# Optimization experiments

Measured on AMD Instinct MI355X. Metric: run time of the kernel, lower is better.

Reference implementation:

```python
import jax, jax.numpy as jnp
import numpy as np
from jax import lax

DROPOUT_RATE = 0.1  # config['dropout']


def setup_inputs() -> dict:
    key = jax.random.key(0)
    kx, kl, kwi, kwh = jax.random.split(key, 4)
    B, T, D, H = 64, 2048, 256, 256
    datamat = jax.random.normal(kx, (B, T, D), dtype=jnp.float32)
    datalens = jax.random.randint(kl, (B,), 1, T + 1, dtype=jnp.int32)
    # OptimizedLSTMCell params: combined input/hidden kernels, gate order (i, f, g, o)
    s_i = 1.0 / np.sqrt(D)
    s_h = 1.0 / np.sqrt(H)
    Wi = jax.random.uniform(kwi, (D, 4 * H), jnp.float32, -s_i, s_i)
    Wh = jax.random.uniform(kwh, (H, 4 * H), jnp.float32, -s_h, s_h)
    b = jnp.zeros((4 * H,), dtype=jnp.float32)
    return {"datamat": datamat, "Wi": Wi, "Wh": Wh, "b": b, "datalens": datalens}


def _dropout(x, rate):
    # training=True dropout with a fixed key (deterministic reference)
    keep = jax.random.bernoulli(jax.random.key(42), 1.0 - rate, x.shape)
    return jnp.where(keep, x / (1.0 - rate), jnp.zeros_like(x))


def _lstm_forward(x, Wi, Wh, b, datalens):
    # x: [B, T, D]
    B, T, D = x.shape
    H = Wh.shape[0]

    def step(carry, xt):
        c, h = carry
        z = xt @ Wi + h @ Wh + b  # [B, 4H], gate order i, f, g, o
        i, f, g, o = jnp.split(z, 4, axis=-1)
        c_new = jax.nn.sigmoid(f) * c + jax.nn.sigmoid(i) * jnp.tanh(g)
        h_new = jax.nn.sigmoid(o) * jnp.tanh(c_new)
        return (c_new, h_new), (c_new, h_new)

    c0 = jnp.zeros((B, H), dtype=x.dtype)
    h0 = jnp.zeros((B, H), dtype=x.dtype)
    _, (cs, hs) = lax.scan(step, (c0, h0), jnp.swapaxes(x, 0, 1))  # [T, B, H] each
    outputs = jnp.swapaxes(hs, 0, 1)  # [B, T, H]
    # flax nn.RNN with seq_lengths + return_carry: select carry at t = len-1 per batch
    idx = jnp.clip(datalens.astype(jnp.int32) - 1, 0, T - 1)  # [B]
    bidx = jnp.arange(B)
    c_last = cs[idx, bidx]  # [B, H]
    h_last = hs[idx, bidx]  # [B, H]
    return (c_last, h_last), outputs


def reference(datamat, Wi, Wh, b, datalens):
    x = _dropout(datamat, DROPOUT_RATE)
    out_carry, outputs = _lstm_forward(x, Wi, Wh, b, datalens)
    return (out_carry, outputs)
```

## Files before the change

### kernel.cpp

```cpp
#include <hip/hip_runtime.h>


typedef __attribute__((ext_vector_type(8))) short short8;
typedef __attribute__((ext_vector_type(4))) float floatx4;
typedef __attribute__((ext_vector_type(4))) int int4v;
typedef __attribute__((ext_vector_type(4))) unsigned short us4;
typedef __attribute__((ext_vector_type(2))) unsigned int uint2v;

#define LOG2E 1.44269504088896f

__device__ __forceinline__ unsigned short f2bf(float f) {
  unsigned int u = __float_as_uint(f);
  u = u + 0x7fffu + ((u >> 16) & 1u);
  return (unsigned short)(u >> 16);
}
__device__ __forceinline__ float fexp2(float x) { return __builtin_amdgcn_exp2f(x); }
__device__ __forceinline__ float frcp(float x) { return __builtin_amdgcn_rcpf(x); }

__device__ __forceinline__ unsigned int tf_bits(unsigned int x0, unsigned int x1) {
  const unsigned int K0 = 0u, K1 = 42u;
  const unsigned int KX = K0 ^ K1 ^ 0x1BD11BDAu;
  x0 += K0; x1 += K1;
#define TF_R(r) { x0 += x1; x1 = (x1 << (r)) | (x1 >> (32 - (r))); x1 ^= x0; }
  TF_R(13) TF_R(15) TF_R(26) TF_R(6)   x0 += K1; x1 += KX + 1u;
  TF_R(17) TF_R(29) TF_R(16) TF_R(24)  x0 += KX; x1 += K0 + 2u;
  TF_R(13) TF_R(15) TF_R(26) TF_R(6)   x0 += K0; x1 += K1 + 3u;
  TF_R(17) TF_R(29) TF_R(16) TF_R(24)  x0 += K1; x1 += KX + 4u;
  TF_R(13) TF_R(15) TF_R(26) TF_R(6)   x0 += KX; x1 += K0 + 5u;
#undef TF_R
  return x0 ^ x1;
}

__global__ __launch_bounds__(256) void k_dropout(const float* __restrict__ x,
                                                 unsigned short* __restrict__ xd) {
  const unsigned int base = (blockIdx.x * 256u + threadIdx.x) * 4u;
  const float4 xv = *reinterpret_cast<const float4*>(x + base);
  const float xs[4] = {xv.x, xv.y, xv.z, xv.w};
  us4 o;
#pragma unroll
  for (int j = 0; j < 4; ++j) {
    const unsigned int bits = tf_bits(0u, base + (unsigned int)j);
    const float u = __uint_as_float((bits >> 9) | 0x3f800000u) - 1.0f;
    const float v = (u < 0.9f) ? (xs[j] / 0.9f) : 0.0f;
    o[j] = f2bf(v);
  }
  *reinterpret_cast<us4*>(xd + base) = o;
}

__global__ __launch_bounds__(256) void k_pack_wi(const float* __restrict__ wi,
                                                 unsigned short* __restrict__ wit) {
  __shared__ float tile[32][33];
  const int k0 = blockIdx.x * 32, n0 = blockIdx.y * 32;
  const int tx = threadIdx.x & 31, ty = threadIdx.x >> 5;
#pragma unroll
  for (int i = 0; i < 4; ++i)
    tile[ty + i * 8][tx] = wi[(k0 + ty + i * 8) * 1024 + n0 + tx];
  __syncthreads();
#pragma unroll
  for (int i = 0; i < 4; ++i)
    wit[(n0 + ty + i * 8) * 256 + k0 + tx] = f2bf(tile[tx][ty + i * 8]);
}

__global__ __launch_bounds__(256) void k_colscale(const float* __restrict__ wh,
                                                  float* __restrict__ dq,
                                                  float* __restrict__ qs) {
  __shared__ float red[256];
  const int t = threadIdx.x;
  const int n = blockIdx.x * 16 + (t & 15);
  const int kg = t >> 4;
  float m = 0.f;
#pragma unroll
  for (int i = 0; i < 16; ++i)
    m = fmaxf(m, fabsf(wh[(kg * 16 + i) * 1024 + n]));
  red[t] = m;
  __syncthreads();
  if (t < 16) {
    const int nn = blockIdx.x * 16 + t;
    float mm = red[t];
#pragma unroll
    for (int j = 1; j < 16; ++j) mm = fmaxf(mm, red[t + j * 16]);
    const float s = (mm > 0.f) ? mm : 1.f;
    const float gsc[4] = {LOG2E, -LOG2E, 2.f * LOG2E, LOG2E};
    dq[nn] = (s / 16129.0f) * gsc[nn >> 8];
    qs[nn] = 127.0f / s;
  }
}

__global__ __launch_bounds__(256) void k_pack_wh_i8(const float* __restrict__ wh,
                                                    const float* __restrict__ qs,
                                                    signed char* __restrict__ wq) {
  const int tid = blockIdx.x * 256 + threadIdx.x;
  const int j = tid & 15, l = (tid >> 4) & 63, kt = (tid >> 10) & 3, ntg = tid >> 12;
  const int k = kt * 64 + ((l >> 4) << 4) + j;
  const int n = ntg * 16 + (l & 15);
  float v = rintf(wh[k * 1024 + n] * qs[n]);
  v = fminf(fmaxf(v, -127.f), 127.f);
  wq[tid] = (signed char)(int)v;
}

__global__ __launch_bounds__(512, 2) void k_fused(
    const unsigned short* __restrict__ xd, const unsigned short* __restrict__ wit,
    const float* __restrict__ bias, unsigned short* __restrict__ xp,
    const signed char* __restrict__ wq, const float* __restrict__ dq,
    const int* __restrict__ lens, float* __restrict__ out,
    unsigned int* __restrict__ flags) {
  __shared__ __align__(16) unsigned short SH[45056];

  const int tid = threadIdx.x, lane = tid & 63;

  if (blockIdx.x >= 32) {
    const int gb = (int)blockIdx.x - 32;
    const int tc = gb >> 9;
    const int rem = gb & 511;
    const int b = rem >> 3, y = rem & 7;
    const int m0 = b * 2048 + tc * 128;

    const int wv = tid >> 6;
    const int wm = wv >> 2;
    const int wn = wv & 3;
    const int srow = tid >> 2, sseg = tid & 3;
    const unsigned short* gA = xd + (m0 + srow) * 256 + sseg * 8;
    const int nsrc = ((srow >> 5) << 8) + y * 32 + (srow & 31);
    const unsigned short* gB = wit + nsrc * 256 + sseg * 8;
    const int soff = srow * 40 + sseg * 8;

    const floatx4 zero4 = {0.f, 0.f, 0.f, 0.f};
    floatx4 acc[4][2];
#pragma unroll
    for (int i = 0; i < 4; ++i) { acc[i][0] = zero4; acc[i][1] = zero4; }

    short8 ra = *(const short8*)(gA);
    short8 rb = *(const short8*)(gB);
    *(short8*)&SH[soff] = ra;
    *(short8*)&SH[10240 + soff] = rb;
    __syncthreads();

    const int frow = (lane & 15) * 40 + ((lane >> 4) << 3);
#pragma unroll 1
    for (int kt = 0; kt < 8; ++kt) {
      const int boff = (kt & 1) * 5120;
      if (kt < 7) {
        ra = *(const short8*)(gA + (kt + 1) * 32);
        rb = *(const short8*)(gB + (kt + 1) * 32);
      }
      short8 af[4], bfv[2];
#pragma unroll
      for (int mt = 0; mt < 4; ++mt)
        af[mt] = *(const short8*)&SH[boff + (wm * 64 + mt * 16) * 40 + frow];
#pragma unroll
      for (int nt = 0; nt < 2; ++nt)
        bfv[nt] = *(const short8*)&SH[10240 + boff + (wn * 32 + nt * 16) * 40 + frow];
#pragma unroll
      for (int mt = 0; mt < 4; ++mt)
#pragma unroll
        for (int nt = 0; nt < 2; ++nt)
          acc[mt][nt] = __builtin_amdgcn_mfma_f32_16x16x32_bf16(af[mt], bfv[nt], acc[mt][nt], 0, 0, 0);
      if (kt < 7) {
        const int noff = boff ^ 5120;
        *(short8*)&SH[noff + soff] = ra;
        *(short8*)&SH[10240 + noff + soff] = rb;
      }
      __syncthreads();
    }

    const float gsc[4] = {LOG2E, -LOG2E, 2.f * LOG2E, LOG2E};
    const float gv = gsc[wn];
    float bv[2];
#pragma unroll
    for (int nt = 0; nt < 2; ++nt)
      bv[nt] = bias[wn * 256 + y * 32 + nt * 16 + (lane & 15)];

    __syncthreads();
#pragma unroll
    for (int mt = 0; mt < 4; ++mt)
#pragma unroll
      for (int nt = 0; nt < 2; ++nt) {
        const int jj = wn * 32 + nt * 16 + (lane & 15);
#pragma unroll
        for (int q = 0; q < 4; ++q) {
          const int row = wm * 64 + mt * 16 + ((lane >> 4) << 2) + q;
          SH[row * 132 + jj] = f2bf((acc[mt][nt][q] + bv[nt]) * gv);
        }
      }
    __syncthreads();

#pragma unroll
    for (int k = 0; k < 8; ++k) {
      const int pi = k * 512 + tid;
      const int row = pi >> 5, u = pi & 31;
      us4 o = {SH[row * 132 + u], SH[row * 132 + 32 + u],
               SH[row * 132 + 64 + u], SH[row * 132 + 96 + u]};
      const int m = m0 + row;
      unsigned short* p = xp + ((size_t)(m & 2047) * 64 + (m >> 11)) * 1024 +
                          (size_t)(y * 32 + u) * 4;
      const uint2v ov = {(unsigned int)(unsigned short)o[0] | ((unsigned int)(unsigned short)o[1] << 16),
                         (unsigned int)(unsigned short)o[2] | ((unsigned int)(unsigned short)o[3] << 16)};
      asm volatile("global_store_dwordx2 %0, %1, off sc0 sc1"
                   :: "v"(p), "v"(ov) : "memory");
    }

    asm volatile("s_waitcnt vmcnt(0)" ::: "memory");
    __syncthreads();
    if (tid == 0) atomicAdd(&flags[tc], 1u);
    return;
  }

  signed char* As = (signed char*)SH;

  const int v = tid >> 6;
  const int wg = (int)blockIdx.x, b0 = wg * 2;

  const int4v zacc = {0, 0, 0, 0};
  ((int4v*)As)[tid] = zacc;

  int4v w[4][2][4];
#pragma unroll
  for (int g = 0; g < 4; ++g)
#pragma unroll
    for (int p = 0; p < 2; ++p)
#pragma unroll
      for (int kt = 0; kt < 4; ++kt) {
        const int ntg = g * 16 + v * 2 + p;
        w[g][p][kt] = *(const int4v*)(wq + (size_t)(((ntg * 4 + kt) * 64 + lane)) * 16);
      }

  const int r = (lane >> 4) & 1;
  const int ph = lane >> 5;
  const int u = v * 32 + ph * 16 + (lane & 15);

  float dq0 = dq[u], dq1 = dq[256 + u], dq2 = dq[512 + u], dq3 = dq[768 + u];
  const int lenm = lens[b0 + r] - 1;
  float c = 0.f, ckeep = 0.f, hkeep = 0.f;

  const signed char* AsR = As + lane * 16;
  signed char* AsW = As + ((u >> 6) * 1024 + (((u >> 4) & 3) * 16 + r * 4) * 16 + (u & 15));

  const char* xpb = (const char*)xp;
  unsigned int xoff = ((unsigned int)(b0 + r) * 1024u + (unsigned int)u * 4u) * 2u;
  char* outb = (char*)(out + 32768);
  unsigned int ooff = ((unsigned int)(b0 + r) * 524288u + (unsigned int)u) * 4u;

  if (tid == 0) {
    while (__hip_atomic_load(&flags[0], __ATOMIC_ACQUIRE, __HIP_MEMORY_SCOPE_AGENT) < 512u)
      __builtin_amdgcn_s_sleep(8);
  }
  __syncthreads();

  uint2 xcur = *(const uint2*)(xpb + xoff);
  xoff += 131072u;
  uint2 xnxt = *(const uint2*)(xpb + xoff);
  xoff += 131072u;

  __syncthreads();

#define GATES(XPAIR, WOFF0, WOFF1)                                              \
  {                                                                             \
    const float xi = __uint_as_float(XPAIR.x << 16);                            \
    const float xf = __uint_as_float(XPAIR.x & 0xffff0000u);                    \
    const float xg = __uint_as_float(XPAIR.y << 16);                            \
    const float xo = __uint_as_float(XPAIR.y & 0xffff0000u);                    \
    const int ai = ph ? acc[0][1][0] : acc[0][0][0];                            \
    const int af_ = ph ? acc[1][1][0] : acc[1][0][0];                           \
    const int ag = ph ? acc[2][1][0] : acc[2][0][0];                            \
    const int ao = ph ? acc[3][1][0] : acc[3][0][0];                            \
    const float zi = fminf(fmaf((float)ai, dq0, xi), 28.85f);                   \
    const float zf = fmaf((float)af_, dq1, xf);                                 \
    const float zg = fminf(fmaf((float)ag, dq2, xg), 57.71f);                   \
    const float zo = fminf(fmaf((float)ao, dq3, xo), 28.85f);                   \
    const float ei = fexp2(zi);                                                 \
    const float e2g = fexp2(zg);                                                \
    const float ef = fexp2(zf);                                                 \
    const float eo = fexp2(zo);                                                 \
    const float p1 = ei * (e2g - 1.f) * frcp((ei + 1.f) * (e2g + 1.f));         \
    const float cn = fmaf(frcp(1.f + ef), c, p1);                               \
    c = cn;                                                                     \
    const float e2c = fexp2(fminf(cn, 15.f) * (2.f * LOG2E));                   \
    const float h = eo * (e2c - 1.f) * frcp((eo + 1.f) * (e2c + 1.f));          \
    const float hm = fmaf(h, 127.f, 12582912.f);                                \
    AsW[WOFF0] = (signed char)__float_as_uint(hm);                              \
    AsW[WOFF1] = (signed char)__float_as_uint(hm);                              \
    *(float*)(outb + ooff) = h;                                                 \
    ooff += 1024u;                                                              \
    if (t_ == lenm) { ckeep = cn; hkeep = h; }                                  \
  }

#define MFMA_BLOCK(O0, O1, O2, O3)                                              \
  int4v acc[4][2];                                                              \
  {                                                                             \
    const int4v a0 = *(const int4v*)(AsR + (O0));                               \
    const int4v a1 = *(const int4v*)(AsR + (O1));                               \
    const int4v a2 = *(const int4v*)(AsR + (O2));                               \
    const int4v a3 = *(const int4v*)(AsR + (O3));                               \
    _Pragma("unroll") for (int g = 0; g < 4; ++g)                               \
    _Pragma("unroll") for (int p = 0; p < 2; ++p) {                             \
      acc[g][p] = __builtin_amdgcn_mfma_i32_16x16x64_i8(a0, w[g][p][0], zacc, 0, 0, 0); \
      acc[g][p] = __builtin_amdgcn_mfma_i32_16x16x64_i8(a1, w[g][p][1], acc[g][p], 0, 0, 0); \
      acc[g][p] = __builtin_amdgcn_mfma_i32_16x16x64_i8(a2, w[g][p][2], acc[g][p], 0, 0, 0); \
      acc[g][p] = __builtin_amdgcn_mfma_i32_16x16x64_i8(a3, w[g][p][3], acc[g][p], 0, 0, 0); \
    }                                                                           \
  }

#pragma unroll 1
  for (int it = 0; it < 1024; ++it) {
    if ((it & 63) == 0) {
      const int ch0 = (it >> 6) + 1;
      const int ch = ch0 < 15 ? ch0 : 15;
      if (tid == 0) {
        while (__hip_atomic_load(&flags[ch], __ATOMIC_ACQUIRE, __HIP_MEMORY_SCOPE_AGENT) < 512u)
          __builtin_amdgcn_s_sleep(8);
      }
      __syncthreads();
    }
    {
      const int t_ = 2 * it;
      const uint2 xpre = *(const uint2*)(xpb + xoff);
      xoff += 131072u;
      MFMA_BLOCK(0, 1024, 2048, 3072)
      GATES(xcur, 4096, 4224)
      xcur = xnxt;
      xnxt = xpre;
      __syncthreads();
    }
    {
      const int t_ = 2 * it + 1;
      const uint2 xpre = *(const uint2*)(xpb + xoff);
      xoff += 131072u;
      MFMA_BLOCK(4096, 5120, 6144, 7168)
      GATES(xcur, 0, 128)
      xcur = xnxt;
      xnxt = xpre;
      __syncthreads();
    }
  }
#undef GATES
#undef MFMA_BLOCK

  out[(size_t)(b0 + r) * 256 + u] = ckeep;
  out[16384 + (size_t)(b0 + r) * 256 + u] = hkeep;
}

extern "C" void kernel_launch(void* const* d_in, const int* in_sizes, int n_in,
                              void* d_out, int out_size, void* d_ws, size_t ws_size,
                              hipStream_t stream) {
  (void)in_sizes; (void)n_in; (void)out_size; (void)ws_size;
  const float* x = (const float*)d_in[0];
  const float* wi = (const float*)d_in[1];
  const float* wh = (const float*)d_in[2];
  const float* bias = (const float*)d_in[3];
  const int* lens = (const int*)d_in[4];
  float* out = (float*)d_out;

  char* ws = (char*)d_ws;
  unsigned short* xd = (unsigned short*)ws;
  unsigned short* xp = (unsigned short*)(ws + 67108864ull);
  unsigned short* wit = (unsigned short*)(ws + 335544320ull);
  float* dq = (float*)(ws + 336068608ull);
  float* qs = (float*)(ws + 336072704ull);
  signed char* wqb = (signed char*)(ws + 336076800ull);
  unsigned int* flags = (unsigned int*)(ws + 336338944ull);

  hipMemsetAsync(flags, 0, 64, stream);
  k_pack_wi<<<dim3(8, 32), 256, 0, stream>>>(wi, wit);
  k_colscale<<<64, 256, 0, stream>>>(wh, dq, qs);
  k_pack_wh_i8<<<1024, 256, 0, stream>>>(wh, qs, wqb);
  k_dropout<<<32768, 256, 0, stream>>>(x, xd);
  k_fused<<<8224, 512, 0, stream>>>(xd, wit, bias, xp, wqb, dq, lens, out, flags);
}
```

Measured before the change: 1.507 ms.

## Fold dropout into fused kernel with per-time-chunk flags and merge prep kernels

```diff
diff --git a/kernel.cpp b/kernel.cpp
--- a/kernel.cpp
+++ b/kernel.cpp
@@ -6,6 +6,7 @@
 typedef __attribute__((ext_vector_type(4))) int int4v;
 typedef __attribute__((ext_vector_type(4))) unsigned short us4;
 typedef __attribute__((ext_vector_type(2))) unsigned int uint2v;
+typedef __attribute__((ext_vector_type(4))) unsigned int uint4v;
 
 #define LOG2E 1.44269504088896f
 
@@ -31,26 +32,37 @@
   return x0 ^ x1;
 }
 
-__global__ __launch_bounds__(256) void k_dropout(const float* __restrict__ x,
-                                                 unsigned short* __restrict__ xd) {
-  const unsigned int base = (blockIdx.x * 256u + threadIdx.x) * 4u;
-  const float4 xv = *reinterpret_cast<const float4*>(x + base);
-  const float xs[4] = {xv.x, xv.y, xv.z, xv.w};
-  us4 o;
-#pragma unroll
-  for (int j = 0; j < 4; ++j) {
-    const unsigned int bits = tf_bits(0u, base + (unsigned int)j);
-    const float u = __uint_as_float((bits >> 9) | 0x3f800000u) - 1.0f;
-    const float v = (u < 0.9f) ? (xs[j] / 0.9f) : 0.0f;
-    o[j] = f2bf(v);
-  }
-  *reinterpret_cast<us4*>(xd + base) = o;
-}
-
-__global__ __launch_bounds__(256) void k_pack_wi(const float* __restrict__ wi,
-                                                 unsigned short* __restrict__ wit) {
+__global__ __launch_bounds__(256) void k_prep(const float* __restrict__ wi,
+                                              const float* __restrict__ wh,
+                                              unsigned short* __restrict__ wit,
+                                              float* __restrict__ dq,
+                                              float* __restrict__ qs) {
+  if (blockIdx.x < 64) {
+    __shared__ float red[256];
+    const int t = threadIdx.x;
+    const int n = blockIdx.x * 16 + (t & 15);
+    const int kg = t >> 4;
+    float m = 0.f;
+#pragma unroll
+    for (int i = 0; i < 16; ++i)
+      m = fmaxf(m, fabsf(wh[(kg * 16 + i) * 1024 + n]));
+    red[t] = m;
+    __syncthreads();
+    if (t < 16) {
+      const int nn = blockIdx.x * 16 + t;
+      float mm = red[t];
+#pragma unroll
+      for (int j = 1; j < 16; ++j) mm = fmaxf(mm, red[t + j * 16]);
+      const float s = (mm > 0.f) ? mm : 1.f;
+      const float gsc[4] = {LOG2E, -LOG2E, 2.f * LOG2E, LOG2E};
+      dq[nn] = (s / 16129.0f) * gsc[nn >> 8];
+      qs[nn] = 127.0f / s;
+    }
+    return;
+  }
   __shared__ float tile[32][33];
-  const int k0 = blockIdx.x * 32, n0 = blockIdx.y * 32;
+  const int idx = (int)blockIdx.x - 64;
+  const int k0 = (idx & 7) * 32, n0 = (idx >> 3) * 32;
   const int tx = threadIdx.x & 31, ty = threadIdx.x >> 5;
 #pragma unroll
   for (int i = 0; i < 4; ++i)
@@ -59,31 +71,6 @@
 #pragma unroll
   for (int i = 0; i < 4; ++i)
     wit[(n0 + ty + i * 8) * 256 + k0 + tx] = f2bf(tile[tx][ty + i * 8]);
-}
-
-__global__ __launch_bounds__(256) void k_colscale(const float* __restrict__ wh,
-                                                  float* __restrict__ dq,
-                                                  float* __restrict__ qs) {
-  __shared__ float red[256];
-  const int t = threadIdx.x;
-  const int n = blockIdx.x * 16 + (t & 15);
-  const int kg = t >> 4;
-  float m = 0.f;
-#pragma unroll
-  for (int i = 0; i < 16; ++i)
-    m = fmaxf(m, fabsf(wh[(kg * 16 + i) * 1024 + n]));
-  red[t] = m;
-  __syncthreads();
-  if (t < 16) {
-    const int nn = blockIdx.x * 16 + t;
-    float mm = red[t];
-#pragma unroll
-    for (int j = 1; j < 16; ++j) mm = fmaxf(mm, red[t + j * 16]);
-    const float s = (mm > 0.f) ? mm : 1.f;
-    const float gsc[4] = {LOG2E, -LOG2E, 2.f * LOG2E, LOG2E};
-    dq[nn] = (s / 16129.0f) * gsc[nn >> 8];
-    qs[nn] = 127.0f / s;
-  }
 }
 
 __global__ __launch_bounds__(256) void k_pack_wh_i8(const float* __restrict__ wh,
@@ -99,21 +86,62 @@
 }
 
 __global__ __launch_bounds__(512, 2) void k_fused(
-    const unsigned short* __restrict__ xd, const unsigned short* __restrict__ wit,
-    const float* __restrict__ bias, unsigned short* __restrict__ xp,
-    const signed char* __restrict__ wq, const float* __restrict__ dq,
-    const int* __restrict__ lens, float* __restrict__ out,
-    unsigned int* __restrict__ flags) {
+    const float* __restrict__ x, unsigned short* __restrict__ xd,
+    const unsigned short* __restrict__ wit, const float* __restrict__ bias,
+    unsigned short* __restrict__ xp, const signed char* __restrict__ wq,
+    const float* __restrict__ dq, const int* __restrict__ lens,
+    float* __restrict__ out, unsigned int* __restrict__ flags) {
   __shared__ __align__(16) unsigned short SH[45056];
 
   const int tid = threadIdx.x, lane = tid & 63;
 
-  if (blockIdx.x >= 32) {
-    const int gb = (int)blockIdx.x - 32;
+  if (blockIdx.x >= 32 && blockIdx.x < 8224) {
+    const int db = (int)blockIdx.x - 32;
+    const int tc = db >> 9, j = db & 511;
+    const int rloc = tid >> 5;
+    const int e0 = (tid & 31) * 8;
+    const int gr = j * 16 + rloc;
+    const int b = gr >> 7, i = gr & 127;
+    const int m = b * 2048 + tc * 128 + i;
+    const unsigned int n0 = (unsigned int)m * 256u + (unsigned int)e0;
+
+    const float4 x0 = *reinterpret_cast<const float4*>(x + (size_t)m * 256 + e0);
+    const float4 x1 = *reinterpret_cast<const float4*>(x + (size_t)m * 256 + e0 + 4);
+    const float xs[8] = {x0.x, x0.y, x0.z, x0.w, x1.x, x1.y, x1.z, x1.w};
+    unsigned short r[8];
+#pragma unroll
+    for (int e = 0; e < 8; ++e) {
+      const unsigned int bits = tf_bits(0u, n0 + (unsigned int)e);
+      const float uu = __uint_as_float((bits >> 9) | 0x3f800000u) - 1.0f;
+      const float vv = (uu < 0.9f) ? (xs[e] / 0.9f) : 0.0f;
+      r[e] = f2bf(vv);
+    }
+    const uint4v ov = {(unsigned int)r[0] | ((unsigned int)r[1] << 16),
+                       (unsigned int)r[2] | ((unsigned int)r[3] << 16),
+                       (unsigned int)r[4] | ((unsigned int)r[5] << 16),
+                       (unsigned int)r[6] | ((unsigned int)r[7] << 16)};
+    unsigned short* p = xd + (size_t)m * 256 + e0;
+    asm volatile("global_store_dwordx4 %0, %1, off sc0 sc1"
+                 :: "v"(p), "v"(ov) : "memory");
+
+    asm volatile("s_waitcnt vmcnt(0)" ::: "memory");
+    __syncthreads();
+    if (tid == 0) atomicAdd(&flags[16 + tc], 1u);
+    return;
+  }
+
+  if (blockIdx.x >= 8224) {
+    const int gb = (int)blockIdx.x - 8224;
     const int tc = gb >> 9;
     const int rem = gb & 511;
     const int b = rem >> 3, y = rem & 7;
     const int m0 = b * 2048 + tc * 128;
+
+    if (tid == 0) {
+      while (__hip_atomic_load(&flags[16 + tc], __ATOMIC_ACQUIRE, __HIP_MEMORY_SCOPE_AGENT) < 512u)
+        __builtin_amdgcn_s_sleep(2);
+    }
+    __syncthreads();
 
     const int wv = tid >> 6;
     const int wm = wv >> 2;
@@ -359,10 +387,8 @@
   signed char* wqb = (signed char*)(ws + 336076800ull);
   unsigned int* flags = (unsigned int*)(ws + 336338944ull);
 
-  hipMemsetAsync(flags, 0, 64, stream);
-  k_pack_wi<<<dim3(8, 32), 256, 0, stream>>>(wi, wit);
-  k_colscale<<<64, 256, 0, stream>>>(wh, dq, qs);
+  hipMemsetAsync(flags, 0, 128, stream);
+  k_prep<<<320, 256, 0, stream>>>(wi, wh, wit, dq, qs);
   k_pack_wh_i8<<<1024, 256, 0, stream>>>(wh, qs, wqb);
-  k_dropout<<<32768, 256, 0, stream>>>(x, xd);
-  k_fused<<<8224, 512, 0, stream>>>(xd, wit, bias, xp, wqb, dq, lens, out, flags);
-}
+  k_fused<<<16416, 512, 0, stream>>>(x, xd, wit, bias, xp, wqb, dq, lens, out, flags);
+}
```

New measurement: 1.732 ms. +15.0%, slower.
